# Kernel optimization log

Measured on AMD Instinct MI355X. Metric: run time of the kernel, lower is better.

The kernel has to match this reference:

```python
import jax, jax.numpy as jnp
import numpy as np

NEG_INF = -1e30  # large negative instead of float('-inf') for fp16/bf16 safety in softmax


def setup_inputs() -> dict:
    key = jax.random.key(0)
    k1, k2, k3, k4 = jax.random.split(key, 4)
    B, T, C, H = 8, 2048, 768, 64
    x = jax.random.normal(k1, (B, T, C), dtype=jnp.float32)
    # nn.Linear(n_embd, head_size, bias=False): y = x @ W.T, W shape (head_size, n_embd)
    s = 1.0 / np.sqrt(C)
    Wk = jax.random.uniform(k2, (H, C), dtype=jnp.float32, minval=-s, maxval=s)
    Wq = jax.random.uniform(k3, (H, C), dtype=jnp.float32, minval=-s, maxval=s)
    Wv = jax.random.uniform(k4, (H, C), dtype=jnp.float32, minval=-s, maxval=s)
    return {"x": x, "Wk": Wk, "Wq": Wq, "Wv": Wv}


def reference(x, Wk, Wq, Wv):
    # x: [B,T,C]; Wk/Wq/Wv: [H,C]
    k = jnp.einsum('btc,hc->bth', x, Wk)  # [B,T,H]
    q = jnp.einsum('btc,hc->bth', x, Wq)
    v = jnp.einsum('btc,hc->bth', x, Wv)
    att = jnp.einsum('bqh,bkh->bqk', q, k)  # [B,T,T], NOTE: no 1/sqrt(H) scaling, faithful to source
    T = x.shape[1]
    causal = jnp.tril(jnp.ones((T, T), dtype=bool))
    att = jnp.where(causal, att, NEG_INF)
    att = jax.nn.softmax(att, axis=-1)
    out = jnp.einsum('bqk,bkh->bqh', att, v)  # [B,T,H]
    return out
```

## Files before the change

kernel.cpp:

```cpp
#include <hip/hip_runtime.h>
#include <hip/hip_bf16.h>
#include <stdint.h>

typedef float    f32x4  __attribute__((ext_vector_type(4)));
typedef float    f32x16 __attribute__((ext_vector_type(16)));
typedef short    s16x8  __attribute__((ext_vector_type(8)));
typedef uint32_t u32x4  __attribute__((ext_vector_type(4)));
typedef uint32_t u32x2  __attribute__((ext_vector_type(2)));

#define NB 8
#define NT 2048
#define NC 768
#define NH 64
#define LOG2E 1.4426950408889634f

__device__ __forceinline__ uint32_t f2bf1(float f) {
  union { float f; uint32_t u; } v; v.f = f;
  uint32_t u = v.u;
  return (u + 0x7fffu + ((u >> 16) & 1u)) >> 16;
}
__device__ __forceinline__ uint32_t packbf2(float lo, float hi) {
  union { __hip_bfloat162 h; uint32_t u; } c;
  c.h = __float22bfloat162_rn(float2{lo, hi});
  return c.u;
}
__device__ __forceinline__ float bf2f(short s) {
  union { float f; uint32_t u; } v; v.u = ((uint32_t)(uint16_t)s) << 16; return v.f;
}

__global__ __launch_bounds__(256) void wconv_kernel(
    const float* __restrict__ Wk, const float* __restrict__ Wq,
    const float* __restrict__ Wv, short* __restrict__ Wf)
{
  int f = blockIdx.x * 256 + threadIdx.x;
  int lane = f & 63;
  int rest = f >> 6;
  int ks = rest % 48;
  int nt = rest / 48;
  int col = lane & 31, half = lane >> 5;
  int n = nt * 32 + col;
  int k = ks * 16 + half * 8;
  const float* src;
  float sc = 1.0f;
  if (n < 64)       { src = Wq + (size_t)n * NC + k; sc = LOG2E; }
  else if (n < 128) { src = Wk + (size_t)(n - 64) * NC + k; }
  else              { src = Wv + (size_t)(n - 128) * NC + k; }
  f32x4 a = *(const f32x4*)src;
  f32x4 b = *(const f32x4*)(src + 4);
  u32x4 o = {packbf2(a[0] * sc, a[1] * sc), packbf2(a[2] * sc, a[3] * sc),
             packbf2(b[0] * sc, b[1] * sc), packbf2(b[2] * sc, b[3] * sc)};
  *(u32x4*)&Wf[(size_t)f * 8] = o;
}

__global__ __launch_bounds__(384, 2) void proj_kernel(
    const float* __restrict__ x, const short* __restrict__ Wf,
    short* __restrict__ qfb, short* __restrict__ kfb, short* __restrict__ vfb)
{
  __shared__ short ldsX[32 * 768];

  const int tid  = threadIdx.x;
  const int lane = tid & 63;
  const int w    = tid >> 6;
  const int col  = lane & 31;
  const int half = lane >> 5;
  const int tg   = blockIdx.x;
  const int t0   = tg * 32;

  {
#pragma unroll
    for (int i = 0; i < 8; ++i) {
      int c   = tid + 384 * i;
      int tok = c / 96, g = c % 96;
      const float* src = x + (size_t)(t0 + tok) * NC + g * 8;
      f32x4 a = *(const f32x4*)src;
      f32x4 d = *(const f32x4*)(src + 4);
      int swz = (g & ~7) | ((g ^ tok) & 7);
      u32x4 o = {packbf2(a[0], a[1]), packbf2(a[2], a[3]),
                 packbf2(d[0], d[1]), packbf2(d[2], d[3])};
      *(u32x4*)&ldsX[tok * 768 + swz * 8] = o;
    }
  }
  __syncthreads();

  f32x16 acc;
#pragma unroll
  for (int e = 0; e < 16; ++e) acc[e] = 0.f;

  const short* wbase = Wf + (((size_t)w * 48) << 9) + lane * 8;
  auto loadW = [&](int ks) -> s16x8 { return *(const s16x8*)(wbase + ((size_t)ks << 9)); };
  auto loadA = [&](int ks) -> s16x8 {
    int grp = ks * 2 + half;
    int swz = (grp & ~7) | ((grp ^ col) & 7);
    return *(const s16x8*)&ldsX[col * 768 + swz * 8];
  };
  {
    s16x8 wA = loadW(0), aA = loadA(0), wB, aB;
#pragma unroll
    for (int ks = 0; ks < 48; ks += 2) {
      wB = loadW(ks + 1); aB = loadA(ks + 1);
      acc = __builtin_amdgcn_mfma_f32_32x32x16_bf16(aA, wA, acc, 0, 0, 0);
      if (ks + 2 < 48) { wA = loadW(ks + 2); aA = loadA(ks + 2); }
      acc = __builtin_amdgcn_mfma_f32_32x32x16_bf16(aB, wB, acc, 0, 0, 0);
    }
  }
  __syncthreads();

  short* scr = ldsX + w * 1088;
  const size_t base = (size_t)tg * 2048;
  if (w < 4) {
#pragma unroll
    for (int r = 0; r < 16; ++r) {
      int rd = (r & 3) + 8 * (r >> 2) + 4 * half;
      scr[rd * 34 + col] = (short)f2bf1(acc[r]);
    }
    short* dst = (w < 2) ? qfb : kfb;
    int ksBase = (w & 1) * 2;
#pragma unroll
    for (int j = 0; j < 2; ++j) {
      s16x8 v = *(const s16x8*)&scr[col * 34 + j * 16 + half * 8];
      *(s16x8*)&dst[base + (ksBase + j) * 512 + lane * 8] = v;
    }
  } else {
#pragma unroll
    for (int r = 0; r < 16; ++r) {
      int rd = (r & 3) + 8 * (r >> 2) + 4 * half;
      scr[col * 34 + rd] = (short)f2bf1(acc[r]);
    }
    int hh = w - 4;
#pragma unroll
    for (int j = 0; j < 2; ++j) {
      s16x8 v = *(const s16x8*)&scr[col * 34 + j * 16 + half * 8];
      *(s16x8*)&vfb[base + (hh * 2 + j) * 512 + lane * 8] = v;
    }
  }
}

__global__ __launch_bounds__(512, 2) void attn_kernel(
    const short* __restrict__ qfb, const short* __restrict__ kfb,
    const short* __restrict__ vfb, float* __restrict__ out)
{
  __shared__ short ldsOb[8 * 32 * 72];
  __shared__ float ldsL[8 * 32];

  const int tid  = threadIdx.x;
  const int lane = tid & 63;
  const int w8   = tid >> 6;
  const int col  = lane & 31;
  const int half = lane >> 5;
  const int b    = blockIdx.x & 7;
  const int p    = blockIdx.x >> 3;

  const short* kfp = kfb + (size_t)b * 64 * 2048 + lane * 8;
  const short* vfp = vfb + (size_t)b * 64 * 2048 + lane * 8;

#define LOADT(K0, K1, K2, K3, V0, V1, V2, V3, TT)            \
  do {                                                       \
    const short* kp_ = kfp + (size_t)(TT) * 2048;            \
    const short* vp_ = vfp + (size_t)(TT) * 2048;            \
    K0 = *(const s16x8*)(kp_);        V0 = *(const s16x8*)(vp_);        \
    K1 = *(const s16x8*)(kp_ + 512);  V1 = *(const s16x8*)(vp_ + 512);  \
    K2 = *(const s16x8*)(kp_ + 1024); V2 = *(const s16x8*)(vp_ + 1024); \
    K3 = *(const s16x8*)(kp_ + 1536); V3 = *(const s16x8*)(vp_ + 1536); \
  } while (0)

#define BODY(K0, K1, K2, K3, V0, V1, V2, V3, TT)                              \
  do {                                                                        \
    f32x16 s_;                                                                \
    _Pragma("unroll") for (int e = 0; e < 16; ++e) s_[e] = 0.f;               \
    __builtin_amdgcn_s_setprio(1);                                            \
    s_ = __builtin_amdgcn_mfma_f32_32x32x16_bf16(K0, qf0, s_, 0, 0, 0);       \
    s_ = __builtin_amdgcn_mfma_f32_32x32x16_bf16(K1, qf1, s_, 0, 0, 0);       \
    s_ = __builtin_amdgcn_mfma_f32_32x32x16_bf16(K2, qf2, s_, 0, 0, 0);       \
    s_ = __builtin_amdgcn_mfma_f32_32x32x16_bf16(K3, qf3, s_, 0, 0, 0);       \
    __builtin_amdgcn_s_setprio(0);                                            \
    if ((TT) == qt) {                                                         \
      _Pragma("unroll") for (int r = 0; r < 16; ++r) {                        \
        int rd_ = (r & 3) + 8 * (r >> 2) + 4 * half;                          \
        if (rd_ > col) s_[r] = -1000.f;           \
      }                                                                       \
    }                                                                         \
    float pp_[16];                                                            \
    float rs_ = 0.f;                                                          \
    _Pragma("unroll") for (int r = 0; r < 16; ++r) {                          \
      pp_[r] = exp2f(s_[r]); rs_ += pp_[r];                                   \
    }                                                                         \
    rs_ += __shfl_xor(rs_, 32);                                               \
    l += rs_;                                                                 \
    uint32_t pw_[8];                                                          \
    _Pragma("unroll") for (int i = 0; i < 8; ++i)                             \
      pw_[i] = packbf2(pp_[2 * i], pp_[2 * i + 1]);                           \
    _Pragma("unroll") for (int kc = 0; kc < 2; ++kc) {                        \
      uint32_t s0_ = half ? pw_[4 * kc]     : pw_[4 * kc + 2];                \
      uint32_t s1_ = half ? pw_[4 * kc + 1] : pw_[4 * kc + 3];                \
      uint32_t r0_ = __shfl_xor(s0_, 32);                                     \
      uint32_t r1_ = __shfl_xor(s1_, 32);                                     \
      uint32_t w0_ = half ? r0_ : pw_[4 * kc];                                \
      uint32_t w1_ = half ? r1_ : pw_[4 * kc + 1];                            \
      uint32_t w2_ = half ? pw_[4 * kc + 2] : r0_;                            \
      uint32_t w3_ = half ? pw_[4 * kc + 3] : r1_;                            \
      union { u32x4 u; s16x8 v; } pf_;                                        \
      pf_.u = (u32x4){w0_, w1_, w2_, w3_};                                    \
      __builtin_amdgcn_s_setprio(1);                                          \
      oa0 = __builtin_amdgcn_mfma_f32_32x32x16_bf16(kc ? V1 : V0, pf_.v, oa0, 0, 0, 0); \
      oa1 = __builtin_amdgcn_mfma_f32_32x32x16_bf16(kc ? V3 : V2, pf_.v, oa1, 0, 0, 0); \
      __builtin_amdgcn_s_setprio(0);                                          \
    }                                                                         \
  } while (0)

#pragma unroll 1
  for (int iter = 0; iter < 2; ++iter) {
    const int qt = iter ? p : 63 - p;
    const int nT = qt + 1;

    s16x8 qf0, qf1, qf2, qf3;
    {
      const short* qp = qfb + (size_t)(b * 64 + qt) * 2048 + lane * 8;
      qf0 = *(const s16x8*)(qp);
      qf1 = *(const s16x8*)(qp + 512);
      qf2 = *(const s16x8*)(qp + 1024);
      qf3 = *(const s16x8*)(qp + 1536);
    }

    f32x16 oa0, oa1;
#pragma unroll
    for (int e = 0; e < 16; ++e) { oa0[e] = 0.f; oa1[e] = 0.f; }
    float l = 0.f;

    s16x8 ka0, ka1, ka2, ka3, va0, va1, va2, va3;
    s16x8 kb0, kb1, kb2, kb3, vb0, vb1, vb2, vb3;

    int t = w8;
    if (t < nT) LOADT(ka0, ka1, ka2, ka3, va0, va1, va2, va3, t);
    if (t + 8 < nT) LOADT(kb0, kb1, kb2, kb3, vb0, vb1, vb2, vb3, t + 8);
    for (; t + 8 < nT; t += 16) {
      BODY(ka0, ka1, ka2, ka3, va0, va1, va2, va3, t);
      if (t + 16 < nT) LOADT(ka0, ka1, ka2, ka3, va0, va1, va2, va3, t + 16);
      BODY(kb0, kb1, kb2, kb3, vb0, vb1, vb2, vb3, t + 8);
      if (t + 24 < nT) LOADT(kb0, kb1, kb2, kb3, vb0, vb1, vb2, vb3, t + 24);
    }
    if (t < nT) BODY(ka0, ka1, ka2, ka3, va0, va1, va2, va3, t);

    if (half == 0) ldsL[w8 * 32 + col] = l;
#pragma unroll
    for (int u = 0; u < 4; ++u) {
      int h0 = 8 * u + 4 * half;
      u32x2 pk0 = {packbf2(oa0[4 * u + 0], oa0[4 * u + 1]),
                   packbf2(oa0[4 * u + 2], oa0[4 * u + 3])};
      *(u32x2*)&ldsOb[(w8 * 32 + col) * 72 + h0] = pk0;
      u32x2 pk1 = {packbf2(oa1[4 * u + 0], oa1[4 * u + 1]),
                   packbf2(oa1[4 * u + 2], oa1[4 * u + 3])};
      *(u32x2*)&ldsOb[(w8 * 32 + col) * 72 + 32 + h0] = pk1;
    }
    __syncthreads();

    {
      const int rr = tid >> 4;
      const int h0 = (tid & 15) * 4;
      float Ls = 0.f;
      float o[4] = {0.f, 0.f, 0.f, 0.f};
#pragma unroll
      for (int s = 0; s < 8; ++s) {
        Ls += ldsL[s * 32 + rr];
        const short* row = &ldsOb[(s * 32 + rr) * 72 + h0];
#pragma unroll
        for (int j = 0; j < 4; ++j) o[j] += bf2f(row[j]);
      }
      float inv = 1.0f / Ls;
      float* ob = out + (size_t)(b * NT + qt * 32 + rr) * NH + h0;
      *(f32x4*)ob = (f32x4){o[0] * inv, o[1] * inv, o[2] * inv, o[3] * inv};
    }
    __syncthreads();
  }
#undef LOADT
#undef BODY
}

extern "C" void kernel_launch(void* const* d_in, const int* in_sizes, int n_in,
                              void* d_out, int out_size, void* d_ws, size_t ws_size,
                              hipStream_t stream) {
  const float* x  = (const float*)d_in[0];
  const float* Wk = (const float*)d_in[1];
  const float* Wq = (const float*)d_in[2];
  const float* Wv = (const float*)d_in[3];
  float* out = (float*)d_out;

  char* ws = (char*)d_ws;
  short* Wf  = (short*)(ws);
  short* qfb = (short*)(ws + (512 << 10));
  short* kfb = (short*)(ws + (512 << 10) + (2 << 20));
  short* vfb = (short*)(ws + (512 << 10) + (4 << 20));

  hipLaunchKernelGGL(wconv_kernel, dim3(72),  dim3(256), 0, stream, Wk, Wq, Wv, Wf);
  hipLaunchKernelGGL(proj_kernel,  dim3(512), dim3(384), 0, stream, x, Wf, qfb, kfb, vfb);
  hipLaunchKernelGGL(attn_kernel,  dim3(256), dim3(512), 0, stream, qfb, kfb, vfb, out);
}
```

Measured before the change: 108.6 us.

## Double token tile per projection block and preload weight fragments in registers

New measurement: 108.8 us. No clear change (+0.2%).

```diff
diff --git a/kernel.cpp b/kernel.cpp
--- a/kernel.cpp
+++ b/kernel.cpp
@@ -14,6 +14,7 @@
 #define NH 64
 #define LOG2E 1.4426950408889634f
 
+
 __device__ __forceinline__ uint32_t f2bf1(float f) {
   union { float f; uint32_t u; } v; v.f = f;
   uint32_t u = v.u;
@@ -28,11 +29,11 @@
   union { float f; uint32_t u; } v; v.u = ((uint32_t)(uint16_t)s) << 16; return v.f;
 }
 
-__global__ __launch_bounds__(256) void wconv_kernel(
+__global__ __launch_bounds__(64) void wconv_kernel(
     const float* __restrict__ Wk, const float* __restrict__ Wq,
     const float* __restrict__ Wv, short* __restrict__ Wf)
 {
-  int f = blockIdx.x * 256 + threadIdx.x;
+  int f = blockIdx.x * 64 + threadIdx.x;
   int lane = f & 63;
   int rest = f >> 6;
   int ks = rest % 48;
@@ -56,83 +57,97 @@
     const float* __restrict__ x, const short* __restrict__ Wf,
     short* __restrict__ qfb, short* __restrict__ kfb, short* __restrict__ vfb)
 {
-  __shared__ short ldsX[32 * 768];
+  extern __shared__ short ldsX[];
 
   const int tid  = threadIdx.x;
   const int lane = tid & 63;
   const int w    = tid >> 6;
   const int col  = lane & 31;
   const int half = lane >> 5;
-  const int tg   = blockIdx.x;
-  const int t0   = tg * 32;
-
-  {
-#pragma unroll
-    for (int i = 0; i < 8; ++i) {
-      int c   = tid + 384 * i;
-      int tok = c / 96, g = c % 96;
-      const float* src = x + (size_t)(t0 + tok) * NC + g * 8;
-      f32x4 a = *(const f32x4*)src;
-      f32x4 d = *(const f32x4*)(src + 4);
-      int swz = (g & ~7) | ((g ^ tok) & 7);
-      u32x4 o = {packbf2(a[0], a[1]), packbf2(a[2], a[3]),
-                 packbf2(d[0], d[1]), packbf2(d[2], d[3])};
-      *(u32x4*)&ldsX[tok * 768 + swz * 8] = o;
-    }
+  const int t0   = blockIdx.x * 64;
+
+#pragma unroll
+  for (int i = 0; i < 16; ++i) {
+    int c   = tid + 384 * i;
+    int tok = c / 96, g = c % 96;
+    const float* src = x + (size_t)(t0 + tok) * NC + g * 8;
+    f32x4 a = *(const f32x4*)src;
+    f32x4 d = *(const f32x4*)(src + 4);
+    int swz = (g & ~7) | ((g ^ tok) & 7);
+    u32x4 o = {packbf2(a[0], a[1]), packbf2(a[2], a[3]),
+               packbf2(d[0], d[1]), packbf2(d[2], d[3])};
+    *(u32x4*)&ldsX[tok * 768 + swz * 8] = o;
   }
+
+  const short* wbase = Wf + (((size_t)w * 48) << 9) + lane * 8;
+#define LDW(KS) (*(const s16x8*)(wbase + ((size_t)(KS) << 9)))
+#define LDA(P, KS) (*(const s16x8*)((P) + \
+    ((((2 * (KS) + half) & ~7) | (((2 * (KS) + half) ^ col) & 7)) * 8)))
+
+  s16x8 W0 = LDW(0), W1 = LDW(1), W2 = LDW(2), W3 = LDW(3),
+        W4 = LDW(4), W5 = LDW(5), W6 = LDW(6), W7 = LDW(7);
   __syncthreads();
 
-  f32x16 acc;
-#pragma unroll
-  for (int e = 0; e < 16; ++e) acc[e] = 0.f;
-
-  const short* wbase = Wf + (((size_t)w * 48) << 9) + lane * 8;
-  auto loadW = [&](int ks) -> s16x8 { return *(const s16x8*)(wbase + ((size_t)ks << 9)); };
-  auto loadA = [&](int ks) -> s16x8 {
-    int grp = ks * 2 + half;
-    int swz = (grp & ~7) | ((grp ^ col) & 7);
-    return *(const s16x8*)&ldsX[col * 768 + swz * 8];
-  };
-  {
-    s16x8 wA = loadW(0), aA = loadA(0), wB, aB;
-#pragma unroll
-    for (int ks = 0; ks < 48; ks += 2) {
-      wB = loadW(ks + 1); aB = loadA(ks + 1);
-      acc = __builtin_amdgcn_mfma_f32_32x32x16_bf16(aA, wA, acc, 0, 0, 0);
-      if (ks + 2 < 48) { wA = loadW(ks + 2); aA = loadA(ks + 2); }
-      acc = __builtin_amdgcn_mfma_f32_32x32x16_bf16(aB, wB, acc, 0, 0, 0);
-    }
+  f32x16 acc0, acc1;
+#pragma unroll
+  for (int e = 0; e < 16; ++e) { acc0[e] = 0.f; acc1[e] = 0.f; }
+
+  const short* ax0 = ldsX + col * 768;
+  const short* ax1 = ldsX + (32 + col) * 768;
+
+#define CHUNK(WR, KS)                                                         \
+  do {                                                                        \
+    s16x8 a0_ = LDA(ax0, KS);                                                 \
+    s16x8 a1_ = LDA(ax1, KS);                                                 \
+    s16x8 nw_;                                                                \
+    if ((KS) + 8 < 48) nw_ = LDW((KS) + 8);      \
+    acc0 = __builtin_amdgcn_mfma_f32_32x32x16_bf16(a0_, WR, acc0, 0, 0, 0);   \
+    acc1 = __builtin_amdgcn_mfma_f32_32x32x16_bf16(a1_, WR, acc1, 0, 0, 0);   \
+    if ((KS) + 8 < 48) WR = nw_;                                              \
+  } while (0)
+
+#pragma unroll
+  for (int k8 = 0; k8 < 48; k8 += 8) {
+    CHUNK(W0, k8 + 0); CHUNK(W1, k8 + 1); CHUNK(W2, k8 + 2); CHUNK(W3, k8 + 3);
+    CHUNK(W4, k8 + 4); CHUNK(W5, k8 + 5); CHUNK(W6, k8 + 6); CHUNK(W7, k8 + 7);
   }
+#undef CHUNK
+#undef LDA
+#undef LDW
+
   __syncthreads();
-
   short* scr = ldsX + w * 1088;
-  const size_t base = (size_t)tg * 2048;
-  if (w < 4) {
-#pragma unroll
-    for (int r = 0; r < 16; ++r) {
-      int rd = (r & 3) + 8 * (r >> 2) + 4 * half;
-      scr[rd * 34 + col] = (short)f2bf1(acc[r]);
-    }
-    short* dst = (w < 2) ? qfb : kfb;
-    int ksBase = (w & 1) * 2;
-#pragma unroll
-    for (int j = 0; j < 2; ++j) {
-      s16x8 v = *(const s16x8*)&scr[col * 34 + j * 16 + half * 8];
-      *(s16x8*)&dst[base + (ksBase + j) * 512 + lane * 8] = v;
-    }
-  } else {
-#pragma unroll
-    for (int r = 0; r < 16; ++r) {
-      int rd = (r & 3) + 8 * (r >> 2) + 4 * half;
-      scr[col * 34 + rd] = (short)f2bf1(acc[r]);
-    }
-    int hh = w - 4;
-#pragma unroll
-    for (int j = 0; j < 2; ++j) {
-      s16x8 v = *(const s16x8*)&scr[col * 34 + j * 16 + half * 8];
-      *(s16x8*)&vfb[base + (hh * 2 + j) * 512 + lane * 8] = v;
-    }
-  }
+
+#define EPI(ACC, TT)                                                          \
+  do {                                                                        \
+    const size_t base_ = ((size_t)blockIdx.x * 2 + (TT)) * 2048;              \
+    if (w < 4) {                                                              \
+      _Pragma("unroll") for (int r = 0; r < 16; ++r) {                        \
+        int rd_ = (r & 3) + 8 * (r >> 2) + 4 * half;           \
+        scr[rd_ * 34 + col] = (short)f2bf1(ACC[r]);                           \
+      }                                                                       \
+      short* dst_ = (w < 2) ? qfb : kfb;                                      \
+      int ksB_ = (w & 1) * 2;                                                 \
+      _Pragma("unroll") for (int j = 0; j < 2; ++j) {                         \
+        s16x8 v_ = *(const s16x8*)&scr[col * 34 + j * 16 + half * 8];         \
+        *(s16x8*)&dst_[base_ + (ksB_ + j) * 512 + lane * 8] = v_;             \
+      }                                                                       \
+    } else {                                                                  \
+      _Pragma("unroll") for (int r = 0; r < 16; ++r) {                        \
+        int rd_ = (r & 3) + 8 * (r >> 2) + 4 * half;         \
+        scr[col * 34 + rd_] = (short)f2bf1(ACC[r]);                           \
+      }                                                                       \
+      int hh_ = w - 4;                                                        \
+      _Pragma("unroll") for (int j = 0; j < 2; ++j) {                         \
+        s16x8 v_ = *(const s16x8*)&scr[col * 34 + j * 16 + half * 8];         \
+        *(s16x8*)&vfb[base_ + (hh_ * 2 + j) * 512 + lane * 8] = v_;           \
+      }                                                                       \
+    }                                                                         \
+  } while (0)
+
+  EPI(acc0, 0);
+  EPI(acc1, 1);
+#undef EPI
 }
 
 __global__ __launch_bounds__(512, 2) void attn_kernel(
@@ -290,7 +305,11 @@
   short* kfb = (short*)(ws + (512 << 10) + (2 << 20));
   short* vfb = (short*)(ws + (512 << 10) + (4 << 20));
 
-  hipLaunchKernelGGL(wconv_kernel, dim3(72),  dim3(256), 0, stream, Wk, Wq, Wv, Wf);
-  hipLaunchKernelGGL(proj_kernel,  dim3(512), dim3(384), 0, stream, x, Wf, qfb, kfb, vfb);
+  hipFuncSetAttribute((const void*)proj_kernel,
+                      hipFuncAttributeMaxDynamicSharedMemorySize, 64 * 768 * 2);
+
+  hipLaunchKernelGGL(wconv_kernel, dim3(288), dim3(64), 0, stream, Wk, Wq, Wv, Wf);
+  hipLaunchKernelGGL(proj_kernel,  dim3(256), dim3(384), 64 * 768 * 2, stream,
+                     x, Wf, qfb, kfb, vfb);
   hipLaunchKernelGGL(attn_kernel,  dim3(256), dim3(512), 0, stream, qfb, kfb, vfb, out);
 }
```
